# Kernel optimization log

Hardware: AMD Instinct MI355X
Metric: run time of the kernel (lower is better)

## Reference

```python
import jax, jax.numpy as jnp
import numpy as np

TOP_K = 2  # k in TopKGate


def setup_inputs() -> dict:
    key = jax.random.key(0)
    k1, k2, k3 = jax.random.split(key, 3)
    B, S, H, E = 4, 2048, 1024, 8
    hidden_states = jax.random.normal(k1, (B, S, H), dtype=jnp.float32)
    Wg = jax.random.normal(k2, (H, E), dtype=jnp.float32) * (H ** -0.5)
    We = jax.random.normal(k3, (E, H, H), dtype=jnp.float32) * (H ** -0.5)
    be = jnp.zeros((E, H), dtype=jnp.float32)
    return {"hidden_states": hidden_states, "Wg": Wg, "We": We, "be": be}


def reference(hidden_states, Wg, We, be):
    # hidden_states: [B, S, H]; Wg: [H, E]; We: [E, H, H]; be: [E, H]
    B, S, H = hidden_states.shape
    T = B * S
    x = hidden_states.reshape(T, H)

    # TopKGate: linear gate -> softmax -> top-k -> renormalize combine weights
    probs = jax.nn.softmax(x @ Wg, axis=-1)              # [T, E]
    top_vals, top_idx = jax.lax.top_k(probs, TOP_K)     # [T, K]
    gates = top_vals / jnp.sum(top_vals, axis=-1, keepdims=True)

    # Experts: run each token through each expert Linear, then gather top-k
    expert_out = jnp.einsum('th,ehd->etd', x, We) + be[:, None, :]  # [E, T, H]
    tok = jnp.arange(T)[:, None]                         # [T, 1]
    sel = expert_out[top_idx, tok, :]                    # [T, K, H]

    # Weighted combine over top-k experts
    out = jnp.sum(gates[..., None] * sel, axis=1)        # [T, H]
    return out.reshape(B, S, H)
```

## Files before the change

### kernel.cpp

```cpp
#include <hip/hip_runtime.h>
#include <hip/hip_bf16.h>

#define H 1024
#define NEXP 8
#define T_TOK 8192
#define CAP 8192
#define TM 128
#define TN 128
#define TPB 16
#define CNTSTRIDE 32
#define NTRANS 2048

typedef __bf16 bf16x8 __attribute__((ext_vector_type(8)));
typedef __bf16 bf16x4 __attribute__((ext_vector_type(4)));
typedef float f32x4 __attribute__((ext_vector_type(4)));

__device__ __forceinline__ void async16(void* lds, const void* g) {
    __builtin_amdgcn_global_load_lds(
        (const __attribute__((address_space(1))) void*)g,
        (__attribute__((address_space(3))) void*)lds, 16, 0, 0);
}

__global__ __launch_bounds__(256) void moe_prep(
    const float* __restrict__ We, __bf16* __restrict__ WeT,
    const float* __restrict__ x, const float* __restrict__ Wg,
    __bf16* __restrict__ Xb, int* __restrict__ cnt,
    int* __restrict__ ltok, float* __restrict__ lgate,
    int* __restrict__ tsel, float* __restrict__ tgate) {
    __shared__ __align__(16) char smem[64 * 65 * 4];
    const int tid = threadIdx.x;

    if (blockIdx.x < NTRANS) {
        float (*t)[65] = (float(*)[65])smem;
        const int tt = blockIdx.x;
        const int e  = tt >> 8;
        const int d0 = ((tt >> 4) & 15) * 64;
        const int h0 = (tt & 15) * 64;
        const int tx = tid & 15;
        const int ty = tid >> 4;
        const float* src = We + ((size_t)e << 20);
        __bf16* dst = WeT + ((size_t)e << 20);
#pragma unroll
        for (int p = 0; p < 4; ++p) {
            const int row = p * 16 + ty;
            const float4 v = *(const float4*)(src + (size_t)(h0 + row) * H + d0 + tx * 4);
            t[row][tx * 4 + 0] = v.x; t[row][tx * 4 + 1] = v.y;
            t[row][tx * 4 + 2] = v.z; t[row][tx * 4 + 3] = v.w;
        }
        __syncthreads();
#pragma unroll
        for (int p = 0; p < 4; ++p) {
            const int drow = p * 16 + ty;
            bf16x4 o;
            o[0] = (__bf16)t[tx * 4 + 0][drow];
            o[1] = (__bf16)t[tx * 4 + 1][drow];
            o[2] = (__bf16)t[tx * 4 + 2][drow];
            o[3] = (__bf16)t[tx * 4 + 3][drow];
            *(bf16x4*)(dst + (size_t)(d0 + drow) * H + h0 + tx * 4) = o;
        }
        return;
    }

    int*   sE    = (int*)smem;
    float* sG    = (float*)(smem + 128);
    int*   lcnt  = (int*)(smem + 256);
    int*   lbase = (int*)(smem + 288);
    int*   lslot = (int*)(smem + 320);
    const int lane = tid & 63;
    const int wave = tid >> 6;
    const int base = (blockIdx.x - NTRANS) * TPB;

    for (int i = 0; i < TPB / 4; ++i) {
        const int tl = wave * (TPB / 4) + i;
        const int t  = base + tl;
        const float* xr  = x  + (size_t)t * H;
        __bf16*      xbr = Xb + (size_t)t * H;
        float a[NEXP];
#pragma unroll
        for (int e = 0; e < NEXP; ++e) a[e] = 0.f;
#pragma unroll
        for (int j = 0; j < H / 256; ++j) {
            const int h = j * 256 + lane * 4;
            const float4 xv = *(const float4*)(xr + h);
            bf16x4 xo;
            xo[0] = (__bf16)xv.x; xo[1] = (__bf16)xv.y;
            xo[2] = (__bf16)xv.z; xo[3] = (__bf16)xv.w;
            *(bf16x4*)(xbr + h) = xo;
            const float xc[4] = {xv.x, xv.y, xv.z, xv.w};
#pragma unroll
            for (int c = 0; c < 4; ++c) {
                const float4 w0 = *(const float4*)(Wg + (h + c) * NEXP);
                const float4 w1 = *(const float4*)(Wg + (h + c) * NEXP + 4);
                a[0] += xc[c] * w0.x; a[1] += xc[c] * w0.y; a[2] += xc[c] * w0.z; a[3] += xc[c] * w0.w;
                a[4] += xc[c] * w1.x; a[5] += xc[c] * w1.y; a[6] += xc[c] * w1.z; a[7] += xc[c] * w1.w;
            }
        }
#pragma unroll
        for (int e = 0; e < NEXP; ++e) {
#pragma unroll
            for (int off = 32; off > 0; off >>= 1)
                a[e] += __shfl_xor(a[e], off, 64);
        }
        int i0 = 0;
#pragma unroll
        for (int e = 1; e < NEXP; ++e) if (a[e] > a[i0]) i0 = e;
        int i1 = (i0 == 0) ? 1 : 0;
#pragma unroll
        for (int e = 0; e < NEXP; ++e) if (e != i0 && a[e] > a[i1]) i1 = e;
        const float ex = __expf(a[i1] - a[i0]);
        const float g0 = 1.f / (1.f + ex);
        const float g1 = ex / (1.f + ex);
        if (lane == 0) {
            sE[tl * 2] = i0; sE[tl * 2 + 1] = i1;
            sG[tl * 2] = g0; sG[tl * 2 + 1] = g1;
        }
    }
    if (tid < NEXP) lcnt[tid] = 0;
    __syncthreads();
    if (tid < TPB * 2) lslot[tid] = atomicAdd(&lcnt[sE[tid]], 1);
    __syncthreads();
    if (tid < NEXP) lbase[tid] = lcnt[tid] ? atomicAdd(&cnt[tid * CNTSTRIDE], lcnt[tid]) : 0;
    __syncthreads();
    if (tid < TPB * 2) {
        const int e = sE[tid];
        const int s = lbase[e] + lslot[tid];
        const int t = base + (tid >> 1);
        ltok[e * CAP + s]  = t;
        lgate[e * CAP + s] = sG[tid];
        tsel[t * 2 + (tid & 1)]  = e * CAP + s;
        tgate[t * 2 + (tid & 1)] = sG[tid];
    }
}

__global__ __launch_bounds__(256) void moe_gemm(
    const __bf16* __restrict__ Xb, const __bf16* __restrict__ WeT,
    const float* __restrict__ be, const int* __restrict__ cnt,
    const int* __restrict__ ltok, const float* __restrict__ lgate,
    __bf16* __restrict__ Eout) {
    const int e  = blockIdx.x & 7;
    const int nt = (blockIdx.x >> 3) & 7;
    const int mt = blockIdx.x >> 6;
    const int ne = cnt[e * CNTSTRIDE];
    const int m0 = mt * TM;
    if (m0 >= ne) return;
    const int n0 = nt * TN;
    int off = 0;
    for (int i2 = 0; i2 < e; ++i2) off += cnt[i2 * CNTSTRIDE];

    __shared__ __align__(16) __bf16 smem[4 * 4096];
    __bf16* Al  = smem;
    __bf16* Al2 = smem + 4096;
    __bf16* Bl  = smem + 8192;
    __bf16* Bl2 = smem + 12288;
    __shared__ int tokL[TM];

    const int tid = threadIdx.x;
    const int lane = tid & 63;
    const int wave = tid >> 6;

    if (tid < TM) {
        const int gi = m0 + tid;
        tokL[tid] = (gi < ne) ? ltok[e * CAP + gi] : 0;
    }
    __syncthreads();

    const __bf16* Bt = WeT + ((size_t)e << 20);
    const int qr = lane >> 4;
    const int rr = lane & 15;
    const int wr = (wave >> 1) * 64;
    const int wc = (wave & 1) * 64;

    f32x4 acc[4][4];
    const f32x4 z = {0.f, 0.f, 0.f, 0.f};
#pragma unroll
    for (int i = 0; i < 4; ++i)
#pragma unroll
        for (int j = 0; j < 4; ++j) acc[i][j] = z;

    const int c0 = tid, c1 = tid + 256;
    const int ar0 = c0 >> 2, ak0 = (((c0 & 3) ^ ((c0 >> 3) & 3)) * 8);
    const int ar1 = c1 >> 2, ak1 = (((c1 & 3) ^ ((c1 >> 3) & 3)) * 8);
    const size_t arow0 = (size_t)tokL[ar0] * H;
    const size_t arow1 = (size_t)tokL[ar1] * H;
    const size_t brow0 = (size_t)(n0 + ar0) * H;
    const size_t brow1 = (size_t)(n0 + ar1) * H;

    for (int k0 = 0; k0 < H; k0 += 64) {
        async16(&Al [c0 * 8], Xb + arow0 + k0 + ak0);
        async16(&Al [c1 * 8], Xb + arow1 + k0 + ak1);
        async16(&Al2[c0 * 8], Xb + arow0 + k0 + 32 + ak0);
        async16(&Al2[c1 * 8], Xb + arow1 + k0 + 32 + ak1);
        async16(&Bl [c0 * 8], Bt + brow0 + k0 + ak0);
        async16(&Bl [c1 * 8], Bt + brow1 + k0 + ak1);
        async16(&Bl2[c0 * 8], Bt + brow0 + k0 + 32 + ak0);
        async16(&Bl2[c1 * 8], Bt + brow1 + k0 + 32 + ak1);
        __syncthreads();
        {
            bf16x8 af[4], bfr[4];
#pragma unroll
            for (int i = 0; i < 4; ++i) {
                const int ra = wr + i * 16 + rr;
                af[i] = *(const bf16x8*)&Al[ra * 32 + ((qr ^ ((ra >> 1) & 3)) * 8)];
            }
#pragma unroll
            for (int j = 0; j < 4; ++j) {
                const int rb = wc + j * 16 + rr;
                bfr[j] = *(const bf16x8*)&Bl[rb * 32 + ((qr ^ ((rb >> 1) & 3)) * 8)];
            }
#pragma unroll
            for (int i = 0; i < 4; ++i)
#pragma unroll
                for (int j = 0; j < 4; ++j)
                    acc[i][j] = __builtin_amdgcn_mfma_f32_16x16x32_bf16(af[i], bfr[j], acc[i][j], 0, 0, 0);
        }
        {
            bf16x8 af[4], bfr[4];
#pragma unroll
            for (int i = 0; i < 4; ++i) {
                const int ra = wr + i * 16 + rr;
                af[i] = *(const bf16x8*)&Al2[ra * 32 + ((qr ^ ((ra >> 1) & 3)) * 8)];
            }
#pragma unroll
            for (int j = 0; j < 4; ++j) {
                const int rb = wc + j * 16 + rr;
                bfr[j] = *(const bf16x8*)&Bl2[rb * 32 + ((qr ^ ((rb >> 1) & 3)) * 8)];
            }
#pragma unroll
            for (int i = 0; i < 4; ++i)
#pragma unroll
                for (int j = 0; j < 4; ++j)
                    acc[i][j] = __builtin_amdgcn_mfma_f32_16x16x32_bf16(af[i], bfr[j], acc[i][j], 0, 0, 0);
        }
        __syncthreads();
    }

    float bev[4];
#pragma unroll
    for (int j = 0; j < 4; ++j) bev[j] = be[e * H + n0 + wc + j * 16 + rr];

    __bf16* Cw = smem + wave * 4096;
#pragma unroll
    for (int i = 0; i < 4; ++i) {
#pragma unroll
        for (int reg = 0; reg < 4; ++reg) {
            const int row = i * 16 + qr * 4 + reg;
            const int key = (row & 7) * 8;
#pragma unroll
            for (int j = 0; j < 4; ++j) {
                const int c = j * 16 + rr;
                Cw[row * 64 + (c ^ key)] = (__bf16)(acc[i][j][reg] + bev[j]);
            }
        }
    }
    const int lrr = lane & 7, lrg = lane >> 3;
#pragma unroll
    for (int p = 0; p < 8; ++p) {
        const int row = p * 8 + lrg;
        const int rglob = m0 + wr + row;
        if (rglob < ne) {
            const int idx8 = ((lrr ^ (row & 7)) * 8);
            const bf16x8 v = *(const bf16x8*)&Cw[row * 64 + idx8];
            *(bf16x8*)(Eout + (size_t)(off + rglob) * H + n0 + wc + lrr * 8) = v;
        }
    }
}

__global__ __launch_bounds__(256) void moe_combine(
    const __bf16* __restrict__ Eout, const int* __restrict__ cnt,
    const int* __restrict__ tsel, const float* __restrict__ tgate,
    float* __restrict__ out) {
    __shared__ int offs[NEXP];
    if (threadIdx.x < NEXP) {
        int o = 0;
        for (int i = 0; i < (int)threadIdx.x; ++i) o += cnt[i * CNTSTRIDE];
        offs[threadIdx.x] = o;
    }
    __syncthreads();
    const int wave = threadIdx.x >> 6, lane = threadIdx.x & 63;
    const int t = blockIdx.x * 4 + wave;
    const int sel0 = tsel[t * 2],  sel1 = tsel[t * 2 + 1];
    const float g0 = tgate[t * 2], g1  = tgate[t * 2 + 1];
    const int e0 = sel0 >> 13, s0 = sel0 & (CAP - 1);
    const int e1 = sel1 >> 13, s1 = sel1 & (CAP - 1);
    const __bf16* r0 = Eout + (size_t)(offs[e0] + s0) * H;
    const __bf16* r1 = Eout + (size_t)(offs[e1] + s1) * H;
    float* orow = out + (size_t)t * H;
#pragma unroll
    for (int c = 0; c < 4; ++c) {
        const int d = c * 256 + lane * 4;
        const bf16x4 a = *(const bf16x4*)(r0 + d);
        const bf16x4 b = *(const bf16x4*)(r1 + d);
        float4 o;
        o.x = g0 * (float)a[0] + g1 * (float)b[0];
        o.y = g0 * (float)a[1] + g1 * (float)b[1];
        o.z = g0 * (float)a[2] + g1 * (float)b[2];
        o.w = g0 * (float)a[3] + g1 * (float)b[3];
        *(float4*)(orow + d) = o;
    }
}

extern "C" void kernel_launch(void* const* d_in, const int* in_sizes, int n_in,
                              void* d_out, int out_size, void* d_ws, size_t ws_size,
                              hipStream_t stream) {
    const float* x  = (const float*)d_in[0];
    const float* Wg = (const float*)d_in[1];
    const float* We = (const float*)d_in[2];
    const float* be = (const float*)d_in[3];
    float* out = (float*)d_out;

    char* ws = (char*)d_ws;
    __bf16* Xb   = (__bf16*)ws;
    __bf16* WeT  = (__bf16*)(ws + ((size_t)16 << 20));
    __bf16* Eout = (__bf16*)(ws + ((size_t)32 << 20));
    char*   meta = ws + ((size_t)64 << 20);
    int*    cnt  = (int*)meta;
    int*    ltok = (int*)(meta + 1024);
    float*  lgat = (float*)(meta + 1024 + (size_t)NEXP * CAP * 4);
    int*    tsel = (int*)(meta + 1024 + (size_t)NEXP * CAP * 8);
    float*  tgat = (float*)(meta + 1024 + (size_t)NEXP * CAP * 8 + (size_t)T_TOK * 8);

    hipMemsetAsync(cnt, 0, NEXP * CNTSTRIDE * sizeof(int), stream);

    moe_prep<<<NTRANS + T_TOK / TPB, 256, 0, stream>>>(We, WeT, x, Wg, Xb, cnt,
                                                       ltok, lgat, tsel, tgat);
    moe_gemm<<<8 * 8 * (T_TOK / TM), 256, 0, stream>>>(Xb, WeT, be, cnt, ltok, lgat, Eout);
    moe_combine<<<T_TOK / 4, 256, 0, stream>>>(Eout, cnt, tsel, tgat, out);
}
```

Baseline: 190.1 us.

## Enlarge MoE GEMM tiles to 256x256 with 4-stage async LDS pipeline

The expert GEMM moves from 128x128 tiles with 256 threads to 256x256 tiles with 512 threads (8 waves, each computing 128x64). The single-buffered K loop becomes a 4-stage ring of LDS buffers with 32-wide K steps, where global-to-LDS async loads for future stages are issued alongside MFMA work and gated by explicit vmcnt waits and raw barriers. MFMA sections are wrapped in s_setprio. The aim is to raise arithmetic intensity and hide load latency, at the cost of 128KB of LDS per block, more padded rows when per-expert counts are not multiples of 256, and fewer blocks in the grid.

```diff
diff --git a/kernel.cpp b/kernel.cpp
--- a/kernel.cpp
+++ b/kernel.cpp
@@ -5,8 +5,6 @@
 #define NEXP 8
 #define T_TOK 8192
 #define CAP 8192
-#define TM 128
-#define TN 128
 #define TPB 16
 #define CNTSTRIDE 32
 #define NTRANS 2048
@@ -20,6 +18,13 @@
         (const __attribute__((address_space(1))) void*)g,
         (__attribute__((address_space(3))) void*)lds, 16, 0, 0);
 }
+
+__device__ __forceinline__ void bar() {
+    asm volatile("" ::: "memory");
+    __builtin_amdgcn_s_barrier();
+    asm volatile("" ::: "memory");
+}
+#define VMCNT(n) asm volatile("s_waitcnt vmcnt(" #n ")" ::: "memory")
 
 __global__ __launch_bounds__(256) void moe_prep(
     const float* __restrict__ We, __bf16* __restrict__ WeT,
@@ -132,33 +137,29 @@
     }
 }
 
-__global__ __launch_bounds__(256) void moe_gemm(
+__global__ __launch_bounds__(512, 2) void moe_gemm(
     const __bf16* __restrict__ Xb, const __bf16* __restrict__ WeT,
     const float* __restrict__ be, const int* __restrict__ cnt,
     const int* __restrict__ ltok, const float* __restrict__ lgate,
     __bf16* __restrict__ Eout) {
     const int e  = blockIdx.x & 7;
-    const int nt = (blockIdx.x >> 3) & 7;
-    const int mt = blockIdx.x >> 6;
+    const int nt = (blockIdx.x >> 3) & 3;
+    const int mt = blockIdx.x >> 5;
     const int ne = cnt[e * CNTSTRIDE];
-    const int m0 = mt * TM;
+    const int m0 = mt * 256;
     if (m0 >= ne) return;
-    const int n0 = nt * TN;
+    const int n0 = nt * 256;
     int off = 0;
     for (int i2 = 0; i2 < e; ++i2) off += cnt[i2 * CNTSTRIDE];
 
-    __shared__ __align__(16) __bf16 smem[4 * 4096];
-    __bf16* Al  = smem;
-    __bf16* Al2 = smem + 4096;
-    __bf16* Bl  = smem + 8192;
-    __bf16* Bl2 = smem + 12288;
-    __shared__ int tokL[TM];
-
-    const int tid = threadIdx.x;
+    __shared__ __align__(16) __bf16 smem[4 * 16384];
+    __shared__ int tokL[256];
+
+    const int tid  = threadIdx.x;
     const int lane = tid & 63;
     const int wave = tid >> 6;
 
-    if (tid < TM) {
+    if (tid < 256) {
         const int gi = m0 + tid;
         tokL[tid] = (gi < ne) ? ltok[e * CAP + gi] : 0;
     }
@@ -167,80 +168,98 @@
     const __bf16* Bt = WeT + ((size_t)e << 20);
     const int qr = lane >> 4;
     const int rr = lane & 15;
-    const int wr = (wave >> 1) * 64;
-    const int wc = (wave & 1) * 64;
-
-    f32x4 acc[4][4];
+    const int wr = (wave >> 2) * 128;
+    const int wc = (wave & 3) * 64;
+    const int ckr = (qr ^ ((rr >> 1) & 3)) * 8;
+
+    const int rA = tid >> 2;
+    const int ck = ((tid & 3) ^ ((tid >> 3) & 3)) * 8;
+    const __bf16* a0p = Xb + (size_t)tokL[rA] * H + ck;
+    const __bf16* a1p = Xb + (size_t)tokL[rA + 128] * H + ck;
+    const __bf16* b0p = Bt + (size_t)(n0 + rA) * H + ck;
+    const __bf16* b1p = Bt + (size_t)(n0 + rA + 128) * H + ck;
+
+    f32x4 acc[8][4];
     const f32x4 z = {0.f, 0.f, 0.f, 0.f};
 #pragma unroll
-    for (int i = 0; i < 4; ++i)
+    for (int i = 0; i < 8; ++i)
 #pragma unroll
         for (int j = 0; j < 4; ++j) acc[i][j] = z;
 
-    const int c0 = tid, c1 = tid + 256;
-    const int ar0 = c0 >> 2, ak0 = (((c0 & 3) ^ ((c0 >> 3) & 3)) * 8);
-    const int ar1 = c1 >> 2, ak1 = (((c1 & 3) ^ ((c1 >> 3) & 3)) * 8);
-    const size_t arow0 = (size_t)tokL[ar0] * H;
-    const size_t arow1 = (size_t)tokL[ar1] * H;
-    const size_t brow0 = (size_t)(n0 + ar0) * H;
-    const size_t brow1 = (size_t)(n0 + ar1) * H;
-
-    for (int k0 = 0; k0 < H; k0 += 64) {
-        async16(&Al [c0 * 8], Xb + arow0 + k0 + ak0);
-        async16(&Al [c1 * 8], Xb + arow1 + k0 + ak1);
-        async16(&Al2[c0 * 8], Xb + arow0 + k0 + 32 + ak0);
-        async16(&Al2[c1 * 8], Xb + arow1 + k0 + 32 + ak1);
-        async16(&Bl [c0 * 8], Bt + brow0 + k0 + ak0);
-        async16(&Bl [c1 * 8], Bt + brow1 + k0 + ak1);
-        async16(&Bl2[c0 * 8], Bt + brow0 + k0 + 32 + ak0);
-        async16(&Bl2[c1 * 8], Bt + brow1 + k0 + 32 + ak1);
-        __syncthreads();
+#pragma unroll
+    for (int t = 0; t < 3; ++t) {
+        __bf16* bb = smem + t * 16384;
+        const int k0 = t * 32;
+        async16(bb +         tid * 8, a0p + k0);
+        async16(bb +  8192 + tid * 8, b0p + k0);
+        async16(bb +  4096 + tid * 8, a1p + k0);
+        async16(bb + 12288 + tid * 8, b1p + k0);
+    }
+    VMCNT(8);
+    bar();
+
+#pragma unroll 4
+    for (int kt = 0; kt < 32; ++kt) {
+        __bf16* bb  = smem + (kt & 3) * 16384;
+        __bf16* bbn = smem + ((kt + 3) & 3) * 16384;
+        const int k3 = (kt + 3) * 32;
+        const bool st = (kt < 29);
         {
             bf16x8 af[4], bfr[4];
 #pragma unroll
-            for (int i = 0; i < 4; ++i) {
-                const int ra = wr + i * 16 + rr;
-                af[i] = *(const bf16x8*)&Al[ra * 32 + ((qr ^ ((ra >> 1) & 3)) * 8)];
+            for (int ii = 0; ii < 4; ++ii)
+                af[ii] = *(const bf16x8*)&bb[(wr + ii * 16 + rr) * 32 + ckr];
+#pragma unroll
+            for (int j = 0; j < 4; ++j)
+                bfr[j] = *(const bf16x8*)&bb[8192 + (wc + j * 16 + rr) * 32 + ckr];
+            if (st) {
+                async16(bbn +        tid * 8, a0p + k3);
+                async16(bbn + 8192 + tid * 8, b0p + k3);
             }
-#pragma unroll
-            for (int j = 0; j < 4; ++j) {
-                const int rb = wc + j * 16 + rr;
-                bfr[j] = *(const bf16x8*)&Bl[rb * 32 + ((qr ^ ((rb >> 1) & 3)) * 8)];
-            }
-#pragma unroll
-            for (int i = 0; i < 4; ++i)
+            bar();
+            __builtin_amdgcn_s_setprio(1);
+#pragma unroll
+            for (int ii = 0; ii < 4; ++ii)
 #pragma unroll
                 for (int j = 0; j < 4; ++j)
-                    acc[i][j] = __builtin_amdgcn_mfma_f32_16x16x32_bf16(af[i], bfr[j], acc[i][j], 0, 0, 0);
+                    acc[ii][j] = __builtin_amdgcn_mfma_f32_16x16x32_bf16(af[ii], bfr[j], acc[ii][j], 0, 0, 0);
+            __builtin_amdgcn_s_setprio(0);
+            bar();
         }
         {
             bf16x8 af[4], bfr[4];
 #pragma unroll
-            for (int i = 0; i < 4; ++i) {
-                const int ra = wr + i * 16 + rr;
-                af[i] = *(const bf16x8*)&Al2[ra * 32 + ((qr ^ ((ra >> 1) & 3)) * 8)];
+            for (int ii = 0; ii < 4; ++ii)
+                af[ii] = *(const bf16x8*)&bb[(wr + (ii + 4) * 16 + rr) * 32 + ckr];
+#pragma unroll
+            for (int j = 0; j < 4; ++j)
+                bfr[j] = *(const bf16x8*)&bb[8192 + (wc + j * 16 + rr) * 32 + ckr];
+            if (st) {
+                async16(bbn +  4096 + tid * 8, a1p + k3);
+                async16(bbn + 12288 + tid * 8, b1p + k3);
             }
-#pragma unroll
-            for (int j = 0; j < 4; ++j) {
-                const int rb = wc + j * 16 + rr;
-                bfr[j] = *(const bf16x8*)&Bl2[rb * 32 + ((qr ^ ((rb >> 1) & 3)) * 8)];
-            }
-#pragma unroll
-            for (int i = 0; i < 4; ++i)
+            bar();
+            __builtin_amdgcn_s_setprio(1);
+#pragma unroll
+            for (int ii = 0; ii < 4; ++ii)
 #pragma unroll
                 for (int j = 0; j < 4; ++j)
-                    acc[i][j] = __builtin_amdgcn_mfma_f32_16x16x32_bf16(af[i], bfr[j], acc[i][j], 0, 0, 0);
-        }
-        __syncthreads();
+                    acc[ii + 4][j] = __builtin_amdgcn_mfma_f32_16x16x32_bf16(af[ii], bfr[j], acc[ii + 4][j], 0, 0, 0);
+            __builtin_amdgcn_s_setprio(0);
+            if (kt < 29)       { VMCNT(8); }
+            else if (kt == 29) { VMCNT(4); }
+            else if (kt == 30) { VMCNT(0); }
+            bar();
+        }
     }
 
     float bev[4];
 #pragma unroll
     for (int j = 0; j < 4; ++j) bev[j] = be[e * H + n0 + wc + j * 16 + rr];
 
-    __bf16* Cw = smem + wave * 4096;
-#pragma unroll
-    for (int i = 0; i < 4; ++i) {
+    __bf16* Cw = smem + wave * 8192;
+#pragma unroll
+    for (int i = 0; i < 8; ++i) {
 #pragma unroll
         for (int reg = 0; reg < 4; ++reg) {
             const int row = i * 16 + qr * 4 + reg;
@@ -254,7 +273,7 @@
     }
     const int lrr = lane & 7, lrg = lane >> 3;
 #pragma unroll
-    for (int p = 0; p < 8; ++p) {
+    for (int p = 0; p < 16; ++p) {
         const int row = p * 8 + lrg;
         const int rglob = m0 + wr + row;
         if (rglob < ne) {
@@ -323,6 +342,6 @@
 
     moe_prep<<<NTRANS + T_TOK / TPB, 256, 0, stream>>>(We, WeT, x, Wg, Xb, cnt,
                                                        ltok, lgat, tsel, tgat);
-    moe_gemm<<<8 * 8 * (T_TOK / TM), 256, 0, stream>>>(Xb, WeT, be, cnt, ltok, lgat, Eout);
+    moe_gemm<<<8 * 4 * (T_TOK / 256), 512, 0, stream>>>(Xb, WeT, be, cnt, ltok, lgat, Eout);
     moe_combine<<<T_TOK / 4, 256, 0, stream>>>(Eout, cnt, tsel, tgat, out);
 }
```

Result: slower. 210.7 us (+10.8%).
